# Kernel tuning notes

Hardware: AMD Instinct MI355X
Metric: run time of the kernel (lower is better)

The kernel has to match this reference:

```python
import jax, jax.numpy as jnp
import numpy as np
from jax import lax

EPS = 1e-8
SLOPE = 0.2

def _modconv(x, wv, W, b, sW, sB, demodulate, pad):
    # StyleGAN2 modulated conv, expressed in the equivalent fused form:
    # scale input by per-sample style s, shared-weight conv, then demodulate output.
    s = wv @ sW.T + sB                                   # [B, Cin]
    y = lax.conv_general_dilated(
        x * s[:, :, None, None], W, (1, 1), [(pad, pad), (pad, pad)],
        dimension_numbers=("NCHW", "OIHW", "NCHW"))      # [B, Cout, H, W]
    if demodulate:
        # d[b,o] = 1/sqrt(sum_{i,k,k} (W[o,i,k,k]*s[b,i])^2 + eps)
        d = lax.rsqrt(jnp.einsum("oihw,bi->bo", W * W, s * s) + EPS)
        y = y * d[:, :, None, None]
    return y + b[None, :, None, None]

def _up2(x):
    B, C, H, W = x.shape
    # matches torch F.interpolate(scale_factor=2, mode='bilinear', align_corners=False)
    return jax.image.resize(x, (B, C, 2 * H, 2 * W), method="bilinear")

def setup_inputs() -> dict:
    B, CIN, COUT, NZ, H = 8, 512, 512, 512, 32
    key = jax.random.key(0)
    ks = jax.random.split(key, 20)
    wscale3 = 1.0 / np.sqrt(CIN * 9)   # kaiming-ish equalized-lr scale baked into weights
    wscale1 = 1.0 / np.sqrt(COUT)
    sscale = 1.0 / np.sqrt(NZ)
    return {
        "maps": jax.random.normal(ks[0], (B, CIN, H, H), jnp.float32),
        "w": jax.random.normal(ks[1], (B, NZ), jnp.float32),
        "rgb": jax.random.normal(ks[2], (B, 3, H, H), jnp.float32),
        "noise0": jax.random.normal(ks[3], (B, 1, 2 * H, 2 * H), jnp.float32),
        "noise1": jax.random.normal(ks[4], (B, 1, 2 * H, 2 * H), jnp.float32),
        "w0": jax.random.normal(ks[5], (COUT, CIN, 3, 3), jnp.float32) * wscale3,
        "b0": jnp.zeros((COUT,), jnp.float32),
        "sW0": jax.random.normal(ks[6], (CIN, NZ), jnp.float32) * sscale,
        "sB0": jnp.ones((CIN,), jnp.float32),
        "ns0": jax.random.normal(ks[7], (COUT,), jnp.float32) * 0.1,
        "w1": jax.random.normal(ks[8], (COUT, COUT, 3, 3), jnp.float32) * wscale3,
        "b1": jnp.zeros((COUT,), jnp.float32),
        "sW1": jax.random.normal(ks[9], (COUT, NZ), jnp.float32) * sscale,
        "sB1": jnp.ones((COUT,), jnp.float32),
        "ns1": jax.random.normal(ks[10], (COUT,), jnp.float32) * 0.1,
        "rgbW": jax.random.normal(ks[11], (3, COUT, 1, 1), jnp.float32) * wscale1,
        "rgbB": jnp.zeros((3,), jnp.float32),
        "rgbSW": jax.random.normal(ks[12], (COUT, NZ), jnp.float32) * sscale,
        "rgbSB": jnp.ones((COUT,), jnp.float32),
    }

def reference(maps, w, rgb, noise0, noise1,
              w0, b0, sW0, sB0, ns0,
              w1, b1, sW1, sB1, ns1,
              rgbW, rgbB, rgbSW, rgbSB):
    rgb = _up2(rgb)
    x = _up2(maps)
    # layer 0: modulated conv 3x3 + noise + leakyrelu
    x = _modconv(x, w, w0, b0, sW0, sB0, True, 1)
    x = x + ns0[None, :, None, None] * noise0
    x = jnp.where(x >= 0, x, SLOPE * x)
    # layer 1
    x = _modconv(x, w, w1, b1, sW1, sB1, True, 1)
    x = x + ns1[None, :, None, None] * noise1
    x = jnp.where(x >= 0, x, SLOPE * x)
    # to_rgb: modulated 1x1 conv, no demodulation
    rgb_out = rgb + _modconv(x, w, rgbW, rgbB, rgbSW, rgbSB, False, 0)
    return (rgb_out, x)
```

## Files before the change

### kernel.cpp

```cpp
#include <hip/hip_runtime.h>

typedef unsigned short u16;
typedef short bf16x8 __attribute__((ext_vector_type(8)));
typedef float f32x4 __attribute__((ext_vector_type(4)));
typedef u16 u16x4 __attribute__((ext_vector_type(4)));
typedef u16 u16x8 __attribute__((ext_vector_type(8)));
typedef unsigned u32x4 __attribute__((ext_vector_type(4)));

__device__ __forceinline__ float b2f(u16 v) {
  union { unsigned u; float f; } x; x.u = ((unsigned)v) << 16; return x.f;
}
__device__ __forceinline__ u16 f2b(float f) {
  unsigned u = __float_as_uint(f);
  unsigned r = (u + 0x7FFFu + ((u >> 16) & 1u)) >> 16;
  return (u16)r;
}
__device__ __forceinline__ float rin(const void* p, size_t i, int bf) {
  return bf ? b2f(((const u16*)p)[i]) : ((const float*)p)[i];
}
__device__ __forceinline__ void async16(const void* g, void* l) {
  __builtin_amdgcn_global_load_lds((const __attribute__((address_space(1))) unsigned*)g,
                                   (__attribute__((address_space(3))) unsigned*)l, 16, 0, 0);
}
__device__ __forceinline__ int detect_bf(const unsigned* __restrict__ w0raw, int tid, int* shflag) {
  if (tid < 64) {
    const unsigned lo = w0raw[tid] & 0xFFFFu;
    const unsigned e = (lo >> 7) & 0xFFu;
    const unsigned long long bad = __ballot(e < 100u || e > 126u);
    if (tid == 0) *shflag = (bad == 0ull) ? 1 : 0;
  }
  __syncthreads();
  return *shflag;
}

__global__ void styleall_kernel(const void* __restrict__ w,
                                const void* __restrict__ sW0, const void* __restrict__ sB0,
                                const void* __restrict__ sW1, const void* __restrict__ sB1,
                                const void* __restrict__ sWR, const void* __restrict__ sBR,
                                float* __restrict__ s0, float* __restrict__ s1,
                                float* __restrict__ sR, const unsigned* __restrict__ w0raw) {
  __shared__ int shflag;
  const int tid = threadIdx.x;
  const int bf = detect_bf(w0raw, tid, &shflag);
  const int mat = blockIdx.z, b = blockIdx.y, oc = blockIdx.x;
  const void* sW = (mat == 0) ? sW0 : ((mat == 1) ? sW1 : sWR);
  const void* sB = (mat == 0) ? sB0 : ((mat == 1) ? sB1 : sBR);
  float* out = (mat == 0) ? s0 : ((mat == 1) ? s1 : sR);
  const int i = oc * 64 + (tid >> 2), q = tid & 3;
  float acc = 0.f;
  if (bf) {
    const u16* rp = (const u16*)sW + (size_t)i * 512 + q * 128;
    const u16* wp = (const u16*)w + b * 512 + q * 128;
    for (int z = 0; z < 128; z += 8) {
      u16x8 a = *(const u16x8*)(rp + z), c = *(const u16x8*)(wp + z);
#pragma unroll
      for (int j = 0; j < 8; ++j) acc += b2f(a[j]) * b2f(c[j]);
    }
  } else {
    const float* rp = (const float*)sW + (size_t)i * 512 + q * 128;
    const float* wp = (const float*)w + b * 512 + q * 128;
    for (int z = 0; z < 128; z += 4) {
      f32x4 a = *(const f32x4*)(rp + z), c = *(const f32x4*)(wp + z);
#pragma unroll
      for (int j = 0; j < 4; ++j) acc += a[j] * c[j];
    }
  }
  acc += __shfl_xor(acc, 1, 64);
  acc += __shfl_xor(acc, 2, 64);
  if (q == 0) out[b * 512 + i] = acc + rin(sB, i, bf);
}

__global__ void demod_kernel(const void* __restrict__ W0, const void* __restrict__ W1,
                             const float* __restrict__ s0, const float* __restrict__ s1,
                             float* __restrict__ dm0, float* __restrict__ dm1,
                             u16* __restrict__ Wp0, u16* __restrict__ Wp1,
                             const unsigned* __restrict__ w0raw) {
  __shared__ int shflag;
  __shared__ float wl[4608];
  __shared__ float wsq[512];
  const int tid = threadIdx.x, lane = tid & 63, wv = tid >> 6;
  const int bf = detect_bf(w0raw, tid, &shflag);
  const int o = blockIdx.x, layer = blockIdx.y;
  const void* W = layer ? W1 : W0;
  const float* s = layer ? s1 : s0;
  float* d = layer ? dm1 : dm0;
  u16* Wp = layer ? Wp1 : Wp0;

  if (bf) {
    const u16* src = (const u16*)W + (size_t)o * 4608;
    for (int e = tid; e < 576; e += 256) {
      u16x8 v = *(const u16x8*)(src + e * 8);
#pragma unroll
      for (int j = 0; j < 8; ++j) wl[e * 8 + j] = b2f(v[j]);
    }
  } else {
    const float* src = (const float*)W + (size_t)o * 4608;
    for (int e = tid; e < 1152; e += 256) {
      f32x4 v = *(const f32x4*)(src + e * 4);
#pragma unroll
      for (int j = 0; j < 4; ++j) wl[e * 4 + j] = v[j];
    }
  }
  __syncthreads();
  for (int i = tid; i < 512; i += 256) {
    float ss = 0.f;
#pragma unroll
    for (int t = 0; t < 9; ++t) {
      const float f = wl[i * 9 + t];
      ss += f * f;
      Wp[t * 262144 + o * 512 + i] = f2b(f);
    }
    wsq[i] = ss;
  }
  __syncthreads();
#pragma unroll
  for (int bb = 0; bb < 2; ++bb) {
    const int b = wv * 2 + bb;
    float part = 0.f;
    for (int i = lane; i < 512; i += 64) { const float sv = s[b * 512 + i]; part += wsq[i] * sv * sv; }
#pragma unroll
    for (int st = 1; st < 64; st <<= 1) part += __shfl_xor(part, st, 64);
    if (lane == 0) d[b * 512 + o] = rsqrtf(part + 1e-8f);
  }
}

__global__ void prep_kernel(u16* __restrict__ actB, u32x4* __restrict__ zr, int NB) {
  const int id = blockIdx.x, tid = threadIdx.x;
  if (id < NB * 65) {
    const int bl = id / 65, sub = id - bl * 65;
    const int c = sub * 256 + tid;
    const int px = c >> 6, seg = c & 63;
    int oy, ox;
    if (px < 66)       { oy = 0;  ox = px; }
    else if (px < 132) { oy = 65; ox = px - 66; }
    else { const int e = px - 132; oy = 1 + (e >> 1); ox = (e & 1) * 65; }
    u32x4 z = {0, 0, 0, 0};
    *(u32x4*)&actB[((size_t)(bl * 4356) + oy * 66 + ox) * 512 + seg * 8] = z;
  } else {
    const int c = (id - NB * 65) * 256 + tid;
    if (c < 24832) { u32x4 z = {0, 0, 0, 0}; zr[c] = z; }
  }
}

__global__ void upsample_kernel(const void* __restrict__ maps, const float* __restrict__ s,
                                void* __restrict__ outb, int b_base,
                                const unsigned* __restrict__ w0raw) {
  __shared__ int shflag;
  __shared__ float it[32][2][33];
  const int tid = threadIdx.x;
  const int bf = detect_bf(w0raw, tid, &shflag);
  const size_t esz = bf ? 2 : 4;
  u16* xg = (u16*)((char*)outb + (98304 + (size_t)(b_base >> 2) * 8388608) * esz);
  int oy, i0, bl;
  if (gridDim.z == 8) {
    const int id = blockIdx.x + (blockIdx.y << 6) + (blockIdx.z << 10);
    bl = id & 7; const int r = id >> 3; oy = r & 63; i0 = (r >> 6) << 5;
  } else {
    oy = blockIdx.x; i0 = blockIdx.y << 5; bl = blockIdx.z;
  }
  const int bg = b_base + bl;
  const int m = oy >> 1;
  int iy0, iy1; float wy0, wy1;
  if ((oy & 1) == 0) { iy0 = (m > 0) ? m - 1 : 0; iy1 = m; wy0 = 0.25f; wy1 = 0.75f; }
  else               { iy0 = m; iy1 = (m < 31) ? m + 1 : 31; wy0 = 0.75f; wy1 = 0.25f; }
#pragma unroll
  for (int k = 0; k < 8; ++k) {
    const int e = tid + k * 256;
    const int c = e >> 6, wsel = (e >> 5) & 1, x = e & 31;
    const int iy = wsel ? iy1 : iy0;
    it[c][wsel][x] = rin(maps, ((size_t)(bg * 512 + i0 + c) * 32 + iy) * 32 + x, bf);
  }
  __syncthreads();
#pragma unroll
  for (int k = 0; k < 8; ++k) {
    const int e = tid + k * 256;
    const int xx = e >> 5, c = e & 31;
    const int mx = xx >> 1;
    int ix0, ix1; float wx0, wx1;
    if ((xx & 1) == 0) { ix0 = (mx > 0) ? mx - 1 : 0; ix1 = mx; wx0 = 0.25f; wx1 = 0.75f; }
    else               { ix0 = mx; ix1 = (mx < 31) ? mx + 1 : 31; wx0 = 0.75f; wx1 = 0.25f; }
    const float r0 = wx0 * it[c][0][ix0] + wx1 * it[c][0][ix1];
    const float r1 = wx0 * it[c][1][ix0] + wx1 * it[c][1][ix1];
    const float v = (wy0 * r0 + wy1 * r1) * s[bg * 512 + i0 + c];
    xg[((size_t)(bl * 4096) + oy * 64 + xx) * 512 + i0 + c] = f2b(v);
  }
}

template <int L>
__global__ __launch_bounds__(512, 2) void conv_kernel(
    void* __restrict__ outb, u16* __restrict__ actBp,
    const u16* __restrict__ Wp, const float* __restrict__ dmod,
    const void* __restrict__ bias, const void* __restrict__ nsc,
    const void* __restrict__ noise, const float* __restrict__ saux,
    const u16* __restrict__ zbuf, const void* __restrict__ rgbW,
    float* __restrict__ rgbacc, int b_base,
    const unsigned* __restrict__ w0raw) {
  __shared__ __attribute__((aligned(16))) u16 lds[65536];
  __shared__ float rgbWl[L == 1 ? 1536 : 4];
  __shared__ int shflag;
  const int tid = threadIdx.x, lane = tid & 63, w = tid >> 6;
  const int bf = detect_bf(w0raw, tid, &shflag);
  const size_t esz = bf ? 2 : 4;

  const int lin = blockIdx.x + (blockIdx.y << 4) + (blockIdx.z << 5);
  const int cpx = (int)(gridDim.z << 2);
  const int wg = (lin & 7) * cpx + (lin >> 3);
  const int bl = wg >> 5, rem = wg & 31;
  const int o0 = (rem >> 4) << 8, n0 = (rem & 15) << 8;
  const int bg = b_base + bl;
  const int wm = w >> 2, wn = w & 3;

  if constexpr (L == 1) {
    for (int e = tid; e < 1536; e += 512) rgbWl[e] = rin(rgbW, e, bf);
  }
  const u16* xg = (const u16*)((const char*)outb +
                  (98304 + (size_t)(b_base >> 2) * 8388608) * esz);

  const int q = lane >> 4, m15 = lane & 15;
  const int lro = m15 * 64 + ((q ^ (lane & 7)) * 8);
  const int srow8 = lane >> 3, schunk = (lane & 7) ^ srow8;
  const size_t aAst = (size_t)(o0 + srow8) * 512 + schunk * 8;

  const int ka0 = (w < 4) ? (2 * w) : (16 + 2 * (w - 4));
  const int ka1 = ka0 + 8;
  const int kbe = (w & 3) * 8 + (w >> 2) * 2;
  const int kb0 = kbe, kb1 = kbe + 1, kb2 = kbe + 4, kb3 = kbe + 5;
  int oyv[4], oxv[4];
  size_t pB[4];
  {
    const int kk4[4] = {kb0, kb1, kb2, kb3};
#pragma unroll
    for (int j = 0; j < 4; ++j) {
      const int p = n0 + kk4[j] * 8 + srow8;
      const int oy = p >> 6, ox = p & 63;
      oyv[j] = oy; oxv[j] = ox;
      pB[j] = ((size_t)bl * 4356 + oy * 66 + ox) * 512 + schunk * 8;
    }
  }

  const u16* bBase[4];
  int koff, aoffu;
  auto setTap = [&](int tn_) {
    const int ty_ = (tn_ * 11) >> 5, tx_ = tn_ - ty_ * 3;
    koff = 0;
    aoffu = tn_ * 262144;
    if constexpr (L == 0) {
#pragma unroll
      for (int j = 0; j < 4; ++j) {
        const int iy_ = oyv[j] + ty_ - 1, ix_ = oxv[j] + tx_ - 1;
        bBase[j] = (((unsigned)iy_ < 64u) & ((unsigned)ix_ < 64u))
          ? (xg + ((size_t)((bl << 12) + (iy_ << 6) + ix_) * 512 + schunk * 8))
          : (zbuf + schunk * 8);
      }
    } else {
      const int sb_ = (ty_ * 66 + tx_) * 512;
#pragma unroll
      for (int j = 0; j < 4; ++j) bBase[j] = actBp + pB[j] + sb_;
    }
  };

#define STAGE_A(k_) \
  async16(Wp + aAst + (size_t)aoffu + (size_t)(k_) * 4096, &lds[stb + (k_) * 512])
#define STAGE_B(j_, k_) \
  async16(bBase[j_] + koff, &lds[stb + 16384 + (k_) * 512])

  f32x4 acc[8][4] = {};
  {
    setTap(0);
    const int stb = 0;
    STAGE_A(ka0); STAGE_A(ka0 + 1);
    STAGE_A(ka1); STAGE_A(ka1 + 1);
    STAGE_B(0, kb0); STAGE_B(1, kb1);
    STAGE_B(2, kb2); STAGE_B(3, kb3);
  }
  koff = 64; aoffu = 64;
  asm volatile("s_waitcnt vmcnt(0)" ::: "memory");
  __builtin_amdgcn_s_barrier();

  int arA  = wm * 8192 + lro;
  int arAx = wm * 8192 + (lro ^ 32);
  int arB  = 16384 + wn * 4096 + lro;
  int arBx = 16384 + wn * 4096 + (lro ^ 32);
  int stb  = 32768;

  bf16x8 afr[4][2], bfA[2][2], bfB[2][2];
#pragma unroll 1
  for (int s = 0; s < 72; ++s) {
    const int s1 = s + 1, ok = (s1 < 72);
    if (ok && (s1 & 7) == 0) setTap(s1 >> 3);

#pragma unroll
    for (int mi = 0; mi < 4; ++mi) {
      afr[mi][0] = *(const bf16x8*)&lds[arA + mi * 1024];
      afr[mi][1] = *(const bf16x8*)&lds[arAx + mi * 1024];
    }
#pragma unroll
    for (int ni = 0; ni < 2; ++ni) {
      bfA[ni][0] = *(const bf16x8*)&lds[arB + ni * 1024];
      bfA[ni][1] = *(const bf16x8*)&lds[arBx + ni * 1024];
      bfB[ni][0] = *(const bf16x8*)&lds[arB + 2048 + ni * 1024];
      bfB[ni][1] = *(const bf16x8*)&lds[arBx + 2048 + ni * 1024];
    }
    if (ok) {
      STAGE_A(ka0); STAGE_A(ka0 + 1);
      STAGE_B(0, kb0); STAGE_B(1, kb1);
      STAGE_B(2, kb2); STAGE_B(3, kb3);
    }
    __builtin_amdgcn_s_setprio(1);
#pragma unroll
    for (int mi = 0; mi < 4; ++mi)
#pragma unroll
      for (int ni = 0; ni < 2; ++ni)
#pragma unroll
        for (int kk = 0; kk < 2; ++kk)
          acc[mi][ni] = __builtin_amdgcn_mfma_f32_16x16x32_bf16(
              afr[mi][kk], bfA[ni][kk], acc[mi][ni], 0, 0, 0);
#pragma unroll
    for (int mi = 0; mi < 4; ++mi)
#pragma unroll
      for (int ni = 0; ni < 2; ++ni)
#pragma unroll
        for (int kk = 0; kk < 2; ++kk)
          acc[mi][2 + ni] = __builtin_amdgcn_mfma_f32_16x16x32_bf16(
              afr[mi][kk], bfB[ni][kk], acc[mi][2 + ni], 0, 0, 0);
    __builtin_amdgcn_s_setprio(0);
    if (ok) { asm volatile("s_waitcnt vmcnt(6)" ::: "memory"); }
    else    { asm volatile("s_waitcnt vmcnt(0)" ::: "memory"); }
    __builtin_amdgcn_s_barrier();

#pragma unroll
    for (int mi = 0; mi < 4; ++mi) {
      afr[mi][0] = *(const bf16x8*)&lds[arA + 4096 + mi * 1024];
      afr[mi][1] = *(const bf16x8*)&lds[arAx + 4096 + mi * 1024];
    }
    if (ok) { STAGE_A(ka1); STAGE_A(ka1 + 1); }
    __builtin_amdgcn_s_setprio(1);
#pragma unroll
    for (int mi = 0; mi < 4; ++mi)
#pragma unroll
      for (int ni = 0; ni < 2; ++ni)
#pragma unroll
        for (int kk = 0; kk < 2; ++kk)
          acc[4 + mi][ni] = __builtin_amdgcn_mfma_f32_16x16x32_bf16(
              afr[mi][kk], bfA[ni][kk], acc[4 + mi][ni], 0, 0, 0);
#pragma unroll
    for (int mi = 0; mi < 4; ++mi)
#pragma unroll
      for (int ni = 0; ni < 2; ++ni)
#pragma unroll
        for (int kk = 0; kk < 2; ++kk)
          acc[4 + mi][2 + ni] = __builtin_amdgcn_mfma_f32_16x16x32_bf16(
              afr[mi][kk], bfB[ni][kk], acc[4 + mi][2 + ni], 0, 0, 0);
    __builtin_amdgcn_s_setprio(0);
    if (ok) { asm volatile("s_waitcnt vmcnt(2)" ::: "memory"); }
    __builtin_amdgcn_s_barrier();

    arA ^= 32768; arAx ^= 32768; arB ^= 32768; arBx ^= 32768; stb ^= 32768;
    koff += 64; aoffu += 64;
  }
#undef STAGE_A
#undef STAGE_B

  if constexpr (L == 0) {
#pragma unroll
    for (int ai = 0; ai < 8; ++ai) {
      const int o = o0 + wm * 128 + ai * 16 + q * 4;
      const f32x4 dv = *(const f32x4*)&dmod[bg * 512 + o];
      const f32x4 sv = *(const f32x4*)&saux[bg * 512 + o];
      float bv[4], nv[4];
#pragma unroll
      for (int r = 0; r < 4; ++r) { bv[r] = rin(bias, o + r, bf); nv[r] = rin(nsc, o + r, bf); }
#pragma unroll
      for (int bj = 0; bj < 4; ++bj) {
        const int p = n0 + wn * 64 + bj * 16 + m15;
        const float np = rin(noise, (size_t)bg * 4096 + p, bf);
        u16x4 pack;
#pragma unroll
        for (int r = 0; r < 4; ++r) {
          float v = acc[ai][bj][r] * dv[r] + bv[r] + nv[r] * np;
          v = (v >= 0.f) ? v : 0.2f * v;
          pack[r] = f2b(v * sv[r]);
        }
        const int oy = p >> 6, ox = p & 63;
        *(u16x4*)&actBp[((size_t)(bl * 4356) + (oy + 1) * 66 + (ox + 1)) * 512 + o] = pack;
      }
    }
  } else {
    char* xreg = (char*)outb + 98304 * esz;
    float racc[4][3] = {};
#pragma unroll
    for (int ai = 0; ai < 8; ++ai) {
      const int o = o0 + wm * 128 + ai * 16 + q * 4;
      const f32x4 dv = *(const f32x4*)&dmod[bg * 512 + o];
      const f32x4 srv = *(const f32x4*)&saux[bg * 512 + o];
      float bv[4], nv[4], w0l[4], w1l[4], w2l[4];
#pragma unroll
      for (int r = 0; r < 4; ++r) {
        bv[r] = rin(bias, o + r, bf); nv[r] = rin(nsc, o + r, bf);
        w0l[r] = rgbWl[o + r]; w1l[r] = rgbWl[512 + o + r]; w2l[r] = rgbWl[1024 + o + r];
      }
#pragma unroll
      for (int bj = 0; bj < 4; ++bj) {
        const int p = n0 + wn * 64 + bj * 16 + m15;
        const float np = rin(noise, (size_t)bg * 4096 + p, bf);
#pragma unroll
        for (int r = 0; r < 4; ++r) {
          float v = acc[ai][bj][r] * dv[r] + bv[r] + nv[r] * np;
          v = (v >= 0.f) ? v : 0.2f * v;
          const size_t xi = (size_t)(bg * 512 + o + r) * 4096 + p;
          if (bf) ((u16*)xreg)[xi] = f2b(v); else ((float*)xreg)[xi] = v;
          const float xr = v * srv[r];
          racc[bj][0] += w0l[r] * xr;
          racc[bj][1] += w1l[r] * xr;
          racc[bj][2] += w2l[r] * xr;
        }
      }
    }
#pragma unroll
    for (int bj = 0; bj < 4; ++bj) {
      const int p = n0 + wn * 64 + bj * 16 + m15;
#pragma unroll
      for (int c = 0; c < 3; ++c) {
        float t = racc[bj][c];
        t += __shfl_xor(t, 16, 64);
        t += __shfl_xor(t, 32, 64);
        if (lane < 16) atomicAdd(&rgbacc[(size_t)(bg * 3 + c) * 4096 + p], t);
      }
    }
  }
}

__global__ void rgbfin_kernel(const float* __restrict__ rgbacc, const void* __restrict__ rgbB,
                              const void* __restrict__ rgb, void* __restrict__ outb,
                              const unsigned* __restrict__ w0raw) {
  __shared__ int shflag;
  const int tid = threadIdx.x;
  const int bf = detect_bf(w0raw, tid, &shflag);
  const int g = blockIdx.x * 256 + tid;
  const int b = g >> 12, p = g & 4095;
  const int oy = p >> 6, ox = p & 63;
  const int m = oy >> 1; int iy0, iy1; float wy0, wy1;
  if ((oy & 1) == 0) { iy0 = (m > 0) ? m - 1 : 0; iy1 = m; wy0 = 0.25f; wy1 = 0.75f; }
  else               { iy0 = m; iy1 = (m < 31) ? m + 1 : 31; wy0 = 0.75f; wy1 = 0.25f; }
  const int mx = ox >> 1; int ix0, ix1; float wx0, wx1;
  if ((ox & 1) == 0) { ix0 = (mx > 0) ? mx - 1 : 0; ix1 = mx; wx0 = 0.25f; wx1 = 0.75f; }
  else               { ix0 = mx; ix1 = (mx < 31) ? mx + 1 : 31; wx0 = 0.75f; wx1 = 0.25f; }
#pragma unroll
  for (int c = 0; c < 3; ++c) {
    const size_t rb = (size_t)(b * 3 + c) * 1024;
    const float up = wy0 * (wx0 * rin(rgb, rb + iy0 * 32 + ix0, bf) + wx1 * rin(rgb, rb + iy0 * 32 + ix1, bf))
                   + wy1 * (wx0 * rin(rgb, rb + iy1 * 32 + ix0, bf) + wx1 * rin(rgb, rb + iy1 * 32 + ix1, bf));
    const float v = up + rin(rgbB, c, bf) + rgbacc[(size_t)(b * 3 + c) * 4096 + p];
    const size_t oi = ((size_t)(b * 3 + c) << 12) + p;
    if (bf) ((u16*)outb)[oi] = f2b(v); else ((float*)outb)[oi] = v;
  }
}


extern "C" void kernel_launch(void* const* d_in, const int* in_sizes, int n_in,
                              void* d_out, int out_size, void* d_ws, size_t ws_size,
                              hipStream_t stream) {
  const void* maps   = d_in[0];
  const void* wlat   = d_in[1];
  const void* rgb    = d_in[2];
  const void* noise0 = d_in[3];
  const void* noise1 = d_in[4];
  const void* w0     = d_in[5];
  const void* b0     = d_in[6];
  const void* sW0    = d_in[7];
  const void* sB0    = d_in[8];
  const void* ns0    = d_in[9];
  const void* w1     = d_in[10];
  const void* b1     = d_in[11];
  const void* sW1    = d_in[12];
  const void* sB1    = d_in[13];
  const void* ns1    = d_in[14];
  const void* rgbW   = d_in[15];
  const void* rgbB   = d_in[16];
  const void* rgbSW  = d_in[17];
  const void* rgbSB  = d_in[18];
  const unsigned* w0raw = (const unsigned*)w0;

  char* ws = (char*)d_ws;
  float* s0     = (float*)(ws + 1024);
  float* s1     = (float*)(ws + 17408);
  float* sR     = (float*)(ws + 33792);
  float* dm0    = (float*)(ws + 50176);
  float* dm1    = (float*)(ws + 66560);
  u16*   zbuf   = (u16*)(ws + 82944);
  float* rgbacc = (float*)(ws + 87040);
  u16*   Wp0    = (u16*)(ws + 480256);
  u16*   Wp1    = (u16*)(ws + 5198848);
  u16*   actB   = (u16*)(ws + 9917440);

  const bool full = ws_size >= (size_t)(9917440 + 35684352);
  const int NB = full ? 8 : 4;

  styleall_kernel<<<dim3(8, 8, 3), 256, 0, stream>>>(wlat, sW0, sB0, sW1, sB1, rgbSW, rgbSB,
                                                     s0, s1, sR, w0raw);
  demod_kernel<<<dim3(512, 2), 256, 0, stream>>>(w0, w1, s0, s1, dm0, dm1, Wp0, Wp1, w0raw);
  prep_kernel<<<NB * 65 + 97, 256, 0, stream>>>(actB, (u32x4*)zbuf, NB);

  for (int pass = 0; pass < 8 / NB; ++pass) {
    const int b_base = pass * NB;
    upsample_kernel<<<dim3(64, 16, NB), 256, 0, stream>>>(maps, s0, d_out, b_base, w0raw);
    conv_kernel<0><<<dim3(16, 2, NB), 512, 0, stream>>>(d_out, actB, Wp0, dm0,
        b0, ns0, noise0, s1, zbuf, nullptr, nullptr, b_base, w0raw);
    conv_kernel<1><<<dim3(16, 2, NB), 512, 0, stream>>>(d_out, actB, Wp1, dm1,
        b1, ns1, noise1, sR, zbuf, rgbW, rgbacc, b_base, w0raw);
  }
  rgbfin_kernel<<<128, 256, 0, stream>>>(rgbacc, rgbB, rgb, d_out, w0raw);
}
```

Before: 432.2 us.

## Shrink conv GEMM tiles to 128x128 with 256-thread blocks for more occupancy

The implicit-GEMM conv kernels now use 128x128 output tiles computed by 4 waves instead of 256x256 tiles by 8 waves. The grid grows from 256 to 1024 blocks, with half the LDS per block and reworked staging and wait counts. The goal is better CU load balance and latency hiding from more resident blocks, at the cost of lower data reuse per tile and more global/L2 traffic for weights and activations.

Result: slower. 512.6 us (+18.6%).

```diff
diff --git a/kernel.cpp b/kernel.cpp
--- a/kernel.cpp
+++ b/kernel.cpp
@@ -187,7 +187,7 @@
 }
 
 template <int L>
-__global__ __launch_bounds__(512, 2) void conv_kernel(
+__global__ __launch_bounds__(256, 2) void conv_kernel(
     void* __restrict__ outb, u16* __restrict__ actBp,
     const u16* __restrict__ Wp, const float* __restrict__ dmod,
     const void* __restrict__ bias, const void* __restrict__ nsc,
@@ -195,23 +195,23 @@
     const u16* __restrict__ zbuf, const void* __restrict__ rgbW,
     float* __restrict__ rgbacc, int b_base,
     const unsigned* __restrict__ w0raw) {
-  __shared__ __attribute__((aligned(16))) u16 lds[65536];
+  __shared__ __attribute__((aligned(16))) u16 lds[32768];
   __shared__ float rgbWl[L == 1 ? 1536 : 4];
   __shared__ int shflag;
   const int tid = threadIdx.x, lane = tid & 63, w = tid >> 6;
   const int bf = detect_bf(w0raw, tid, &shflag);
   const size_t esz = bf ? 2 : 4;
 
-  const int lin = blockIdx.x + (blockIdx.y << 4) + (blockIdx.z << 5);
-  const int cpx = (int)(gridDim.z << 2);
+  const int lin = blockIdx.x + (blockIdx.y << 5) + (blockIdx.z << 7);
+  const int cpx = (int)(gridDim.z << 4);
   const int wg = (lin & 7) * cpx + (lin >> 3);
-  const int bl = wg >> 5, rem = wg & 31;
-  const int o0 = (rem >> 4) << 8, n0 = (rem & 15) << 8;
+  const int bl = wg >> 7, rem = wg & 127;
+  const int o0 = (rem >> 5) << 7, n0 = (rem & 31) << 7;
   const int bg = b_base + bl;
-  const int wm = w >> 2, wn = w & 3;
+  const int wm = w >> 1, wn = w & 1;
 
   if constexpr (L == 1) {
-    for (int e = tid; e < 1536; e += 512) rgbWl[e] = rin(rgbW, e, bf);
+    for (int e = tid; e < 1536; e += 256) rgbWl[e] = rin(rgbW, e, bf);
   }
   const u16* xg = (const u16*)((const char*)outb +
                   (98304 + (size_t)(b_base >> 2) * 8388608) * esz);
@@ -221,14 +221,11 @@
   const int srow8 = lane >> 3, schunk = (lane & 7) ^ srow8;
   const size_t aAst = (size_t)(o0 + srow8) * 512 + schunk * 8;
 
-  const int ka0 = (w < 4) ? (2 * w) : (16 + 2 * (w - 4));
-  const int ka1 = ka0 + 8;
-  const int kbe = (w & 3) * 8 + (w >> 2) * 2;
-  const int kb0 = kbe, kb1 = kbe + 1, kb2 = kbe + 4, kb3 = kbe + 5;
+  const int sbase = (w & 1) * 2 + (w >> 1) * 8;
   int oyv[4], oxv[4];
   size_t pB[4];
   {
-    const int kk4[4] = {kb0, kb1, kb2, kb3};
+    const int kk4[4] = {sbase, sbase + 1, sbase + 4, sbase + 5};
 #pragma unroll
     for (int j = 0; j < 4; ++j) {
       const int p = n0 + kk4[j] * 8 + srow8;
@@ -262,100 +259,84 @@
 #define STAGE_A(k_) \
   async16(Wp + aAst + (size_t)aoffu + (size_t)(k_) * 4096, &lds[stb + (k_) * 512])
 #define STAGE_B(j_, k_) \
-  async16(bBase[j_] + koff, &lds[stb + 16384 + (k_) * 512])
-
-  f32x4 acc[8][4] = {};
+  async16(bBase[j_] + koff, &lds[stb + 8192 + (k_) * 512])
+
+  f32x4 acc[4][4] = {};
   {
     setTap(0);
     const int stb = 0;
-    STAGE_A(ka0); STAGE_A(ka0 + 1);
-    STAGE_A(ka1); STAGE_A(ka1 + 1);
-    STAGE_B(0, kb0); STAGE_B(1, kb1);
-    STAGE_B(2, kb2); STAGE_B(3, kb3);
+    STAGE_A(sbase); STAGE_A(sbase + 1);
+    STAGE_A(sbase + 4); STAGE_A(sbase + 5);
+    STAGE_B(0, sbase); STAGE_B(1, sbase + 1);
+    STAGE_B(2, sbase + 4); STAGE_B(3, sbase + 5);
   }
   koff = 64; aoffu = 64;
   asm volatile("s_waitcnt vmcnt(0)" ::: "memory");
   __builtin_amdgcn_s_barrier();
 
-  int arA  = wm * 8192 + lro;
-  int arAx = wm * 8192 + (lro ^ 32);
-  int arB  = 16384 + wn * 4096 + lro;
-  int arBx = 16384 + wn * 4096 + (lro ^ 32);
-  int stb  = 32768;
-
-  bf16x8 afr[4][2], bfA[2][2], bfB[2][2];
+  int arA  = wm * 4096 + lro;
+  int arAx = wm * 4096 + (lro ^ 32);
+  int arB  = 8192 + wn * 4096 + lro;
+  int arBx = 8192 + wn * 4096 + (lro ^ 32);
+  int stb  = 16384;
+
+  bf16x8 afr[2][2], bfr[4][2];
 #pragma unroll 1
   for (int s = 0; s < 72; ++s) {
     const int s1 = s + 1, ok = (s1 < 72);
     if (ok && (s1 & 7) == 0) setTap(s1 >> 3);
 
 #pragma unroll
-    for (int mi = 0; mi < 4; ++mi) {
+    for (int ni = 0; ni < 4; ++ni) {
+      bfr[ni][0] = *(const bf16x8*)&lds[arB + ni * 1024];
+      bfr[ni][1] = *(const bf16x8*)&lds[arBx + ni * 1024];
+    }
+#pragma unroll
+    for (int mi = 0; mi < 2; ++mi) {
       afr[mi][0] = *(const bf16x8*)&lds[arA + mi * 1024];
       afr[mi][1] = *(const bf16x8*)&lds[arAx + mi * 1024];
     }
-#pragma unroll
-    for (int ni = 0; ni < 2; ++ni) {
-      bfA[ni][0] = *(const bf16x8*)&lds[arB + ni * 1024];
-      bfA[ni][1] = *(const bf16x8*)&lds[arBx + ni * 1024];
-      bfB[ni][0] = *(const bf16x8*)&lds[arB + 2048 + ni * 1024];
-      bfB[ni][1] = *(const bf16x8*)&lds[arBx + 2048 + ni * 1024];
-    }
     if (ok) {
-      STAGE_A(ka0); STAGE_A(ka0 + 1);
-      STAGE_B(0, kb0); STAGE_B(1, kb1);
-      STAGE_B(2, kb2); STAGE_B(3, kb3);
+      STAGE_A(sbase); STAGE_A(sbase + 1);
+      STAGE_B(0, sbase); STAGE_B(1, sbase + 1);
     }
     __builtin_amdgcn_s_setprio(1);
 #pragma unroll
-    for (int mi = 0; mi < 4; ++mi)
-#pragma unroll
-      for (int ni = 0; ni < 2; ++ni)
+    for (int mi = 0; mi < 2; ++mi)
+#pragma unroll
+      for (int ni = 0; ni < 4; ++ni)
 #pragma unroll
         for (int kk = 0; kk < 2; ++kk)
           acc[mi][ni] = __builtin_amdgcn_mfma_f32_16x16x32_bf16(
-              afr[mi][kk], bfA[ni][kk], acc[mi][ni], 0, 0, 0);
-#pragma unroll
-    for (int mi = 0; mi < 4; ++mi)
-#pragma unroll
-      for (int ni = 0; ni < 2; ++ni)
-#pragma unroll
-        for (int kk = 0; kk < 2; ++kk)
-          acc[mi][2 + ni] = __builtin_amdgcn_mfma_f32_16x16x32_bf16(
-              afr[mi][kk], bfB[ni][kk], acc[mi][2 + ni], 0, 0, 0);
+              afr[mi][kk], bfr[ni][kk], acc[mi][ni], 0, 0, 0);
     __builtin_amdgcn_s_setprio(0);
-    if (ok) { asm volatile("s_waitcnt vmcnt(6)" ::: "memory"); }
+    if (ok) { asm volatile("s_waitcnt vmcnt(4)" ::: "memory"); }
     else    { asm volatile("s_waitcnt vmcnt(0)" ::: "memory"); }
     __builtin_amdgcn_s_barrier();
 
 #pragma unroll
-    for (int mi = 0; mi < 4; ++mi) {
-      afr[mi][0] = *(const bf16x8*)&lds[arA + 4096 + mi * 1024];
-      afr[mi][1] = *(const bf16x8*)&lds[arAx + 4096 + mi * 1024];
-    }
-    if (ok) { STAGE_A(ka1); STAGE_A(ka1 + 1); }
+    for (int mi = 0; mi < 2; ++mi) {
+      afr[mi][0] = *(const bf16x8*)&lds[arA + 2048 + mi * 1024];
+      afr[mi][1] = *(const bf16x8*)&lds[arAx + 2048 + mi * 1024];
+    }
+    if (ok) {
+      STAGE_B(2, sbase + 4); STAGE_B(3, sbase + 5);
+      STAGE_A(sbase + 4); STAGE_A(sbase + 5);
+    }
     __builtin_amdgcn_s_setprio(1);
 #pragma unroll
-    for (int mi = 0; mi < 4; ++mi)
-#pragma unroll
-      for (int ni = 0; ni < 2; ++ni)
+    for (int mi = 0; mi < 2; ++mi)
+#pragma unroll
+      for (int ni = 0; ni < 4; ++ni)
 #pragma unroll
         for (int kk = 0; kk < 2; ++kk)
-          acc[4 + mi][ni] = __builtin_amdgcn_mfma_f32_16x16x32_bf16(
-              afr[mi][kk], bfA[ni][kk], acc[4 + mi][ni], 0, 0, 0);
-#pragma unroll
-    for (int mi = 0; mi < 4; ++mi)
-#pragma unroll
-      for (int ni = 0; ni < 2; ++ni)
-#pragma unroll
-        for (int kk = 0; kk < 2; ++kk)
-          acc[4 + mi][2 + ni] = __builtin_amdgcn_mfma_f32_16x16x32_bf16(
-              afr[mi][kk], bfB[ni][kk], acc[4 + mi][2 + ni], 0, 0, 0);
+          acc[2 + mi][ni] = __builtin_amdgcn_mfma_f32_16x16x32_bf16(
+              afr[mi][kk], bfr[ni][kk], acc[2 + mi][ni], 0, 0, 0);
     __builtin_amdgcn_s_setprio(0);
     if (ok) { asm volatile("s_waitcnt vmcnt(2)" ::: "memory"); }
     __builtin_amdgcn_s_barrier();
 
-    arA ^= 32768; arAx ^= 32768; arB ^= 32768; arBx ^= 32768; stb ^= 32768;
+    arA ^= 16384; arAx ^= 16384; arB ^= 16384; arBx ^= 16384; stb ^= 16384;
     koff += 64; aoffu += 64;
   }
 #undef STAGE_A
@@ -363,8 +344,8 @@
 
   if constexpr (L == 0) {
 #pragma unroll
-    for (int ai = 0; ai < 8; ++ai) {
-      const int o = o0 + wm * 128 + ai * 16 + q * 4;
+    for (int ai = 0; ai < 4; ++ai) {
+      const int o = o0 + wm * 64 + ai * 16 + q * 4;
       const f32x4 dv = *(const f32x4*)&dmod[bg * 512 + o];
       const f32x4 sv = *(const f32x4*)&saux[bg * 512 + o];
       float bv[4], nv[4];
@@ -389,8 +370,8 @@
     char* xreg = (char*)outb + 98304 * esz;
     float racc[4][3] = {};
 #pragma unroll
-    for (int ai = 0; ai < 8; ++ai) {
-      const int o = o0 + wm * 128 + ai * 16 + q * 4;
+    for (int ai = 0; ai < 4; ++ai) {
+      const int o = o0 + wm * 64 + ai * 16 + q * 4;
       const f32x4 dv = *(const f32x4*)&dmod[bg * 512 + o];
       const f32x4 srv = *(const f32x4*)&saux[bg * 512 + o];
       float bv[4], nv[4], w0l[4], w1l[4], w2l[4];
@@ -504,9 +485,9 @@
   for (int pass = 0; pass < 8 / NB; ++pass) {
     const int b_base = pass * NB;
     upsample_kernel<<<dim3(64, 16, NB), 256, 0, stream>>>(maps, s0, d_out, b_base, w0raw);
-    conv_kernel<0><<<dim3(16, 2, NB), 512, 0, stream>>>(d_out, actB, Wp0, dm0,
+    conv_kernel<0><<<dim3(32, 4, NB), 256, 0, stream>>>(d_out, actB, Wp0, dm0,
         b0, ns0, noise0, s1, zbuf, nullptr, nullptr, b_base, w0raw);
-    conv_kernel<1><<<dim3(16, 2, NB), 512, 0, stream>>>(d_out, actB, Wp1, dm1,
+    conv_kernel<1><<<dim3(32, 4, NB), 256, 0, stream>>>(d_out, actB, Wp1, dm1,
         b1, ns1, noise1, sR, zbuf, rgbW, rgbacc, b_base, w0raw);
   }
   rgbfin_kernel<<<128, 256, 0, stream>>>(rgbacc, rgbB, rgb, d_out, w0raw);
```

## Switch conv GEMM main loop from 16x16x32 to 32x32x16 MFMA tiles

Applied to the files above, without the earlier changes.

Replaces the 16x16x32 bf16 MFMA micro-tiling with 32x32x16 MFMA instructions that accumulate into 16-wide vectors. LDS fragment reads, the swizzled column offsets, the waitcnt counts and both epilogues (layer-0 activation write and layer-1 x/rgb accumulation) are remapped to the new accumulator layout. The larger MFMA shape is meant to cut LDS reads and instruction count per FLOP. It changes the swizzle read pattern, so it risks LDS bank conflicts and higher register pressure.

Result: slower. 556.0 us (+28.6%).

```diff
diff --git a/kernel.cpp b/kernel.cpp
--- a/kernel.cpp
+++ b/kernel.cpp
@@ -3,6 +3,7 @@
 typedef unsigned short u16;
 typedef short bf16x8 __attribute__((ext_vector_type(8)));
 typedef float f32x4 __attribute__((ext_vector_type(4)));
+typedef float f32x16 __attribute__((ext_vector_type(16)));
 typedef u16 u16x4 __attribute__((ext_vector_type(4)));
 typedef u16 u16x8 __attribute__((ext_vector_type(8)));
 typedef unsigned u32x4 __attribute__((ext_vector_type(4)));
@@ -216,8 +217,10 @@
   const u16* xg = (const u16*)((const char*)outb +
                   (98304 + (size_t)(b_base >> 2) * 8388608) * esz);
 
-  const int q = lane >> 4, m15 = lane & 15;
-  const int lro = m15 * 64 + ((q ^ (lane & 7)) * 8);
+  const int h = lane >> 5, l7 = lane & 7, l31 = lane & 31;
+  int co[4];
+#pragma unroll
+  for (int kq = 0; kq < 4; ++kq) co[kq] = ((((kq << 1) | h) ^ l7) << 3);
   const int srow8 = lane >> 3, schunk = (lane & 7) ^ srow8;
   const size_t aAst = (size_t)(o0 + srow8) * 512 + schunk * 8;
 
@@ -264,7 +267,7 @@
 #define STAGE_B(j_, k_) \
   async16(bBase[j_] + koff, &lds[stb + 16384 + (k_) * 512])
 
-  f32x4 acc[8][4] = {};
+  f32x16 acc[4][2] = {};
   {
     setTap(0);
     const int stb = 0;
@@ -277,29 +280,25 @@
   asm volatile("s_waitcnt vmcnt(0)" ::: "memory");
   __builtin_amdgcn_s_barrier();
 
-  int arA  = wm * 8192 + lro;
-  int arAx = wm * 8192 + (lro ^ 32);
-  int arB  = 16384 + wn * 4096 + lro;
-  int arBx = 16384 + wn * 4096 + (lro ^ 32);
-  int stb  = 32768;
-
-  bf16x8 afr[4][2], bfA[2][2], bfB[2][2];
+  int arA = wm * 8192 + l31 * 64;
+  int arB = 16384 + wn * 4096 + l31 * 64;
+  int stb = 32768;
+
+  bf16x8 afr[2][4], bfr[2][4];
 #pragma unroll 1
   for (int s = 0; s < 72; ++s) {
     const int s1 = s + 1, ok = (s1 < 72);
     if (ok && (s1 & 7) == 0) setTap(s1 >> 3);
 
 #pragma unroll
-    for (int mi = 0; mi < 4; ++mi) {
-      afr[mi][0] = *(const bf16x8*)&lds[arA + mi * 1024];
-      afr[mi][1] = *(const bf16x8*)&lds[arAx + mi * 1024];
-    }
-#pragma unroll
-    for (int ni = 0; ni < 2; ++ni) {
-      bfA[ni][0] = *(const bf16x8*)&lds[arB + ni * 1024];
-      bfA[ni][1] = *(const bf16x8*)&lds[arBx + ni * 1024];
-      bfB[ni][0] = *(const bf16x8*)&lds[arB + 2048 + ni * 1024];
-      bfB[ni][1] = *(const bf16x8*)&lds[arBx + 2048 + ni * 1024];
+    for (int kq = 0; kq < 4; ++kq) {
+      bfr[0][kq] = *(const bf16x8*)&lds[arB + co[kq]];
+      bfr[1][kq] = *(const bf16x8*)&lds[arB + 2048 + co[kq]];
+    }
+#pragma unroll
+    for (int kq = 0; kq < 4; ++kq) {
+      afr[0][kq] = *(const bf16x8*)&lds[arA + co[kq]];
+      afr[1][kq] = *(const bf16x8*)&lds[arA + 2048 + co[kq]];
     }
     if (ok) {
       STAGE_A(ka0); STAGE_A(ka0 + 1);
@@ -308,54 +307,38 @@
     }
     __builtin_amdgcn_s_setprio(1);
 #pragma unroll
-    for (int mi = 0; mi < 4; ++mi)
-#pragma unroll
-      for (int ni = 0; ni < 2; ++ni)
-#pragma unroll
-        for (int kk = 0; kk < 2; ++kk)
-          acc[mi][ni] = __builtin_amdgcn_mfma_f32_16x16x32_bf16(
-              afr[mi][kk], bfA[ni][kk], acc[mi][ni], 0, 0, 0);
-#pragma unroll
-    for (int mi = 0; mi < 4; ++mi)
-#pragma unroll
-      for (int ni = 0; ni < 2; ++ni)
-#pragma unroll
-        for (int kk = 0; kk < 2; ++kk)
-          acc[mi][2 + ni] = __builtin_amdgcn_mfma_f32_16x16x32_bf16(
-              afr[mi][kk], bfB[ni][kk], acc[mi][2 + ni], 0, 0, 0);
+    for (int kq = 0; kq < 4; ++kq)
+#pragma unroll
+      for (int mi = 0; mi < 2; ++mi)
+#pragma unroll
+        for (int ni = 0; ni < 2; ++ni)
+          acc[mi][ni] = __builtin_amdgcn_mfma_f32_32x32x16_bf16(
+              afr[mi][kq], bfr[ni][kq], acc[mi][ni], 0, 0, 0);
     __builtin_amdgcn_s_setprio(0);
-    if (ok) { asm volatile("s_waitcnt vmcnt(6)" ::: "memory"); }
+    if (ok) { asm volatile("s_waitcnt vmcnt(4)" ::: "memory"); }
     else    { asm volatile("s_waitcnt vmcnt(0)" ::: "memory"); }
     __builtin_amdgcn_s_barrier();
 
 #pragma unroll
-    for (int mi = 0; mi < 4; ++mi) {
-      afr[mi][0] = *(const bf16x8*)&lds[arA + 4096 + mi * 1024];
-      afr[mi][1] = *(const bf16x8*)&lds[arAx + 4096 + mi * 1024];
+    for (int kq = 0; kq < 4; ++kq) {
+      afr[0][kq] = *(const bf16x8*)&lds[arA + 4096 + co[kq]];
+      afr[1][kq] = *(const bf16x8*)&lds[arA + 6144 + co[kq]];
     }
     if (ok) { STAGE_A(ka1); STAGE_A(ka1 + 1); }
     __builtin_amdgcn_s_setprio(1);
 #pragma unroll
-    for (int mi = 0; mi < 4; ++mi)
-#pragma unroll
-      for (int ni = 0; ni < 2; ++ni)
-#pragma unroll
-        for (int kk = 0; kk < 2; ++kk)
-          acc[4 + mi][ni] = __builtin_amdgcn_mfma_f32_16x16x32_bf16(
-              afr[mi][kk], bfA[ni][kk], acc[4 + mi][ni], 0, 0, 0);
-#pragma unroll
-    for (int mi = 0; mi < 4; ++mi)
-#pragma unroll
-      for (int ni = 0; ni < 2; ++ni)
-#pragma unroll
-        for (int kk = 0; kk < 2; ++kk)
-          acc[4 + mi][2 + ni] = __builtin_amdgcn_mfma_f32_16x16x32_bf16(
-              afr[mi][kk], bfB[ni][kk], acc[4 + mi][2 + ni], 0, 0, 0);
+    for (int kq = 0; kq < 4; ++kq)
+#pragma unroll
+      for (int mi = 0; mi < 2; ++mi)
+#pragma unroll
+        for (int ni = 0; ni < 2; ++ni)
+          acc[2 + mi][ni] = __builtin_amdgcn_mfma_f32_32x32x16_bf16(
+              afr[mi][kq], bfr[ni][kq], acc[2 + mi][ni], 0, 0, 0);
     __builtin_amdgcn_s_setprio(0);
     if (ok) { asm volatile("s_waitcnt vmcnt(2)" ::: "memory"); }
     __builtin_amdgcn_s_barrier();
 
-    arA ^= 32768; arAx ^= 32768; arB ^= 32768; arBx ^= 32768; stb ^= 32768;
+    arA ^= 32768; arB ^= 32768; stb ^= 32768;
     koff += 64; aoffu += 64;
   }
 #undef STAGE_A
@@ -363,68 +346,79 @@
 
   if constexpr (L == 0) {
 #pragma unroll
-    for (int ai = 0; ai < 8; ++ai) {
-      const int o = o0 + wm * 128 + ai * 16 + q * 4;
-      const f32x4 dv = *(const f32x4*)&dmod[bg * 512 + o];
-      const f32x4 sv = *(const f32x4*)&saux[bg * 512 + o];
-      float bv[4], nv[4];
-#pragma unroll
-      for (int r = 0; r < 4; ++r) { bv[r] = rin(bias, o + r, bf); nv[r] = rin(nsc, o + r, bf); }
-#pragma unroll
-      for (int bj = 0; bj < 4; ++bj) {
-        const int p = n0 + wn * 64 + bj * 16 + m15;
+    for (int mi = 0; mi < 4; ++mi) {
+      f32x4 dvv[4], svv[4]; float bvv[4][4], nvv[4][4];
+#pragma unroll
+      for (int g = 0; g < 4; ++g) {
+        const int o = o0 + wm * 128 + mi * 32 + g * 8 + h * 4;
+        dvv[g] = *(const f32x4*)&dmod[bg * 512 + o];
+        svv[g] = *(const f32x4*)&saux[bg * 512 + o];
+#pragma unroll
+        for (int r = 0; r < 4; ++r) { bvv[g][r] = rin(bias, o + r, bf); nvv[g][r] = rin(nsc, o + r, bf); }
+      }
+#pragma unroll
+      for (int ni = 0; ni < 2; ++ni) {
+        const int p = n0 + wn * 64 + ni * 32 + l31;
         const float np = rin(noise, (size_t)bg * 4096 + p, bf);
-        u16x4 pack;
-#pragma unroll
-        for (int r = 0; r < 4; ++r) {
-          float v = acc[ai][bj][r] * dv[r] + bv[r] + nv[r] * np;
-          v = (v >= 0.f) ? v : 0.2f * v;
-          pack[r] = f2b(v * sv[r]);
+        const int oy = p >> 6, ox = p & 63;
+        u16* wbase = &actBp[((size_t)(bl * 4356) + (oy + 1) * 66 + (ox + 1)) * 512];
+#pragma unroll
+        for (int g = 0; g < 4; ++g) {
+          const int o = o0 + wm * 128 + mi * 32 + g * 8 + h * 4;
+          u16x4 pack;
+#pragma unroll
+          for (int r = 0; r < 4; ++r) {
+            float v = acc[mi][ni][g * 4 + r] * dvv[g][r] + bvv[g][r] + nvv[g][r] * np;
+            v = (v >= 0.f) ? v : 0.2f * v;
+            pack[r] = f2b(v * svv[g][r]);
+          }
+          *(u16x4*)&wbase[o] = pack;
         }
-        const int oy = p >> 6, ox = p & 63;
-        *(u16x4*)&actBp[((size_t)(bl * 4356) + (oy + 1) * 66 + (ox + 1)) * 512 + o] = pack;
       }
     }
   } else {
     char* xreg = (char*)outb + 98304 * esz;
-    float racc[4][3] = {};
-#pragma unroll
-    for (int ai = 0; ai < 8; ++ai) {
-      const int o = o0 + wm * 128 + ai * 16 + q * 4;
-      const f32x4 dv = *(const f32x4*)&dmod[bg * 512 + o];
-      const f32x4 srv = *(const f32x4*)&saux[bg * 512 + o];
-      float bv[4], nv[4], w0l[4], w1l[4], w2l[4];
-#pragma unroll
-      for (int r = 0; r < 4; ++r) {
-        bv[r] = rin(bias, o + r, bf); nv[r] = rin(nsc, o + r, bf);
-        w0l[r] = rgbWl[o + r]; w1l[r] = rgbWl[512 + o + r]; w2l[r] = rgbWl[1024 + o + r];
+    float racc[2][3] = {};
+#pragma unroll
+    for (int mi = 0; mi < 4; ++mi) {
+      f32x4 dvv[4], srv[4]; float bvv[4][4], nvv[4][4];
+#pragma unroll
+      for (int g = 0; g < 4; ++g) {
+        const int o = o0 + wm * 128 + mi * 32 + g * 8 + h * 4;
+        dvv[g] = *(const f32x4*)&dmod[bg * 512 + o];
+        srv[g] = *(const f32x4*)&saux[bg * 512 + o];
+#pragma unroll
+        for (int r = 0; r < 4; ++r) { bvv[g][r] = rin(bias, o + r, bf); nvv[g][r] = rin(nsc, o + r, bf); }
       }
 #pragma unroll
-      for (int bj = 0; bj < 4; ++bj) {
-        const int p = n0 + wn * 64 + bj * 16 + m15;
+      for (int ni = 0; ni < 2; ++ni) {
+        const int p = n0 + wn * 64 + ni * 32 + l31;
         const float np = rin(noise, (size_t)bg * 4096 + p, bf);
 #pragma unroll
-        for (int r = 0; r < 4; ++r) {
-          float v = acc[ai][bj][r] * dv[r] + bv[r] + nv[r] * np;
-          v = (v >= 0.f) ? v : 0.2f * v;
-          const size_t xi = (size_t)(bg * 512 + o + r) * 4096 + p;
-          if (bf) ((u16*)xreg)[xi] = f2b(v); else ((float*)xreg)[xi] = v;
-          const float xr = v * srv[r];
-          racc[bj][0] += w0l[r] * xr;
-          racc[bj][1] += w1l[r] * xr;
-          racc[bj][2] += w2l[r] * xr;
+        for (int g = 0; g < 4; ++g) {
+          const int o = o0 + wm * 128 + mi * 32 + g * 8 + h * 4;
+#pragma unroll
+          for (int r = 0; r < 4; ++r) {
+            float v = acc[mi][ni][g * 4 + r] * dvv[g][r] + bvv[g][r] + nvv[g][r] * np;
+            v = (v >= 0.f) ? v : 0.2f * v;
+            const size_t xi = (size_t)(bg * 512 + o + r) * 4096 + p;
+            if (bf) ((u16*)xreg)[xi] = f2b(v); else ((float*)xreg)[xi] = v;
+            const float xr = v * srv[g][r];
+            racc[ni][0] += rgbWl[o + r] * xr;
+            racc[ni][1] += rgbWl[512 + o + r] * xr;
+            racc[ni][2] += rgbWl[1024 + o + r] * xr;
+          }
         }
       }
     }
 #pragma unroll
-    for (int bj = 0; bj < 4; ++bj) {
-      const int p = n0 + wn * 64 + bj * 16 + m15;
+    for (int ni = 0; ni < 2; ++ni) {
+      const int p = n0 + wn * 64 + ni * 32 + l31;
 #pragma unroll
       for (int c = 0; c < 3; ++c) {
-        float t = racc[bj][c];
-        t += __shfl_xor(t, 16, 64);
+        float t = racc[ni][c];
         t += __shfl_xor(t, 32, 64);
-        if (lane < 16) atomicAdd(&rgbacc[(size_t)(bg * 3 + c) * 4096 + p], t);
+        if (lane < 32) atomicAdd(&rgbacc[(size_t)(bg * 3 + c) * 4096 + p], t);
       }
     }
   }
```

## Load conv weight fragments directly from global memory, staging only activations in LDS

Applied to the files above, without the earlier changes.

The weight (A) operand is no longer staged through LDS. Each wave loads its MFMA A fragments straight from global memory (L2-cached weights), and only the activation tile is double-buffered in LDS, which halves LDS use and drops one barrier per step. The aim is to cut LDS traffic and synchronisation and possibly raise occupancy. The cost is that global-load latency now sits directly in front of the MFMAs, and the 16-byte fragment loads are only partly coalesced, with just a vmcnt(0) wait protecting them.

Result: slower. 824.6 us (+90.8%).

```diff
diff --git a/kernel.cpp b/kernel.cpp
--- a/kernel.cpp
+++ b/kernel.cpp
@@ -195,7 +195,7 @@
     const u16* __restrict__ zbuf, const void* __restrict__ rgbW,
     float* __restrict__ rgbacc, int b_base,
     const unsigned* __restrict__ w0raw) {
-  __shared__ __attribute__((aligned(16))) u16 lds[65536];
+  __shared__ __attribute__((aligned(16))) u16 lds[32768];
   __shared__ float rgbWl[L == 1 ? 1536 : 4];
   __shared__ int shflag;
   const int tid = threadIdx.x, lane = tid & 63, w = tid >> 6;
@@ -219,10 +219,9 @@
   const int q = lane >> 4, m15 = lane & 15;
   const int lro = m15 * 64 + ((q ^ (lane & 7)) * 8);
   const int srow8 = lane >> 3, schunk = (lane & 7) ^ srow8;
-  const size_t aAst = (size_t)(o0 + srow8) * 512 + schunk * 8;
-
-  const int ka0 = (w < 4) ? (2 * w) : (16 + 2 * (w - 4));
-  const int ka1 = ka0 + 8;
+
+  const u16* aG = Wp + (size_t)(o0 + wm * 128 + m15) * 512 + q * 8;
+
   const int kbe = (w & 3) * 8 + (w >> 2) * 2;
   const int kb0 = kbe, kb1 = kbe + 1, kb2 = kbe + 4, kb3 = kbe + 5;
   int oyv[4], oxv[4];
@@ -239,11 +238,10 @@
   }
 
   const u16* bBase[4];
-  int koff, aoffu;
+  int koff;
   auto setTap = [&](int tn_) {
     const int ty_ = (tn_ * 11) >> 5, tx_ = tn_ - ty_ * 3;
     koff = 0;
-    aoffu = tn_ * 262144;
     if constexpr (L == 0) {
 #pragma unroll
       for (int j = 0; j < 4; ++j) {
@@ -259,106 +257,95 @@
     }
   };
 
-#define STAGE_A(k_) \
-  async16(Wp + aAst + (size_t)aoffu + (size_t)(k_) * 4096, &lds[stb + (k_) * 512])
 #define STAGE_B(j_, k_) \
-  async16(bBase[j_] + koff, &lds[stb + 16384 + (k_) * 512])
+  async16(bBase[j_] + koff, &lds[stb + (k_) * 512])
 
   f32x4 acc[8][4] = {};
+  int stb = 0;
   {
     setTap(0);
-    const int stb = 0;
-    STAGE_A(ka0); STAGE_A(ka0 + 1);
-    STAGE_A(ka1); STAGE_A(ka1 + 1);
     STAGE_B(0, kb0); STAGE_B(1, kb1);
     STAGE_B(2, kb2); STAGE_B(3, kb3);
   }
-  koff = 64; aoffu = 64;
+  koff = 64;
   asm volatile("s_waitcnt vmcnt(0)" ::: "memory");
   __builtin_amdgcn_s_barrier();
 
-  int arA  = wm * 8192 + lro;
-  int arAx = wm * 8192 + (lro ^ 32);
-  int arB  = 16384 + wn * 4096 + lro;
-  int arBx = 16384 + wn * 4096 + (lro ^ 32);
-  int stb  = 32768;
-
-  bf16x8 afr[4][2], bfA[2][2], bfB[2][2];
+  int arB  = wn * 4096 + lro;
+  int arBx = wn * 4096 + (lro ^ 32);
+  stb = 16384;
+
+  bf16x8 afr0[4], afr1[4], bfr[4][2];
 #pragma unroll 1
   for (int s = 0; s < 72; ++s) {
     const int s1 = s + 1, ok = (s1 < 72);
     if (ok && (s1 & 7) == 0) setTap(s1 >> 3);
-
-#pragma unroll
-    for (int mi = 0; mi < 4; ++mi) {
-      afr[mi][0] = *(const bf16x8*)&lds[arA + mi * 1024];
-      afr[mi][1] = *(const bf16x8*)&lds[arAx + mi * 1024];
-    }
-#pragma unroll
-    for (int ni = 0; ni < 2; ++ni) {
-      bfA[ni][0] = *(const bf16x8*)&lds[arB + ni * 1024];
-      bfA[ni][1] = *(const bf16x8*)&lds[arBx + ni * 1024];
-      bfB[ni][0] = *(const bf16x8*)&lds[arB + 2048 + ni * 1024];
-      bfB[ni][1] = *(const bf16x8*)&lds[arBx + 2048 + ni * 1024];
-    }
+    const int aCur = (s >> 3) * 262144 + (s & 7) * 64;
+
+#pragma unroll
+    for (int mi = 0; mi < 4; ++mi)
+      afr0[mi] = *(const bf16x8*)(aG + aCur + mi * 8192);
+#pragma unroll
+    for (int mi = 0; mi < 4; ++mi)
+      afr1[mi] = *(const bf16x8*)(aG + aCur + mi * 8192 + 32);
+
+#pragma unroll
+    for (int ni = 0; ni < 4; ++ni) {
+      bfr[ni][0] = *(const bf16x8*)&lds[arB + ni * 1024];
+      bfr[ni][1] = *(const bf16x8*)&lds[arBx + ni * 1024];
+    }
+
     if (ok) {
-      STAGE_A(ka0); STAGE_A(ka0 + 1);
       STAGE_B(0, kb0); STAGE_B(1, kb1);
       STAGE_B(2, kb2); STAGE_B(3, kb3);
     }
+
     __builtin_amdgcn_s_setprio(1);
 #pragma unroll
     for (int mi = 0; mi < 4; ++mi)
 #pragma unroll
-      for (int ni = 0; ni < 2; ++ni)
-#pragma unroll
-        for (int kk = 0; kk < 2; ++kk)
-          acc[mi][ni] = __builtin_amdgcn_mfma_f32_16x16x32_bf16(
-              afr[mi][kk], bfA[ni][kk], acc[mi][ni], 0, 0, 0);
-#pragma unroll
-    for (int mi = 0; mi < 4; ++mi)
-#pragma unroll
-      for (int ni = 0; ni < 2; ++ni)
-#pragma unroll
-        for (int kk = 0; kk < 2; ++kk)
-          acc[mi][2 + ni] = __builtin_amdgcn_mfma_f32_16x16x32_bf16(
-              afr[mi][kk], bfB[ni][kk], acc[mi][2 + ni], 0, 0, 0);
+      for (int ni = 0; ni < 4; ++ni)
+        acc[mi][ni] = __builtin_amdgcn_mfma_f32_16x16x32_bf16(
+            afr0[mi], bfr[ni][0], acc[mi][ni], 0, 0, 0);
     __builtin_amdgcn_s_setprio(0);
-    if (ok) { asm volatile("s_waitcnt vmcnt(6)" ::: "memory"); }
-    else    { asm volatile("s_waitcnt vmcnt(0)" ::: "memory"); }
-    __builtin_amdgcn_s_barrier();
-
-#pragma unroll
-    for (int mi = 0; mi < 4; ++mi) {
-      afr[mi][0] = *(const bf16x8*)&lds[arA + 4096 + mi * 1024];
-      afr[mi][1] = *(const bf16x8*)&lds[arAx + 4096 + mi * 1024];
-    }
-    if (ok) { STAGE_A(ka1); STAGE_A(ka1 + 1); }
+#pragma unroll
+    for (int mi = 0; mi < 4; ++mi)
+      afr0[mi] = *(const bf16x8*)(aG + aCur + (4 + mi) * 8192);
+
     __builtin_amdgcn_s_setprio(1);
 #pragma unroll
     for (int mi = 0; mi < 4; ++mi)
 #pragma unroll
-      for (int ni = 0; ni < 2; ++ni)
-#pragma unroll
-        for (int kk = 0; kk < 2; ++kk)
-          acc[4 + mi][ni] = __builtin_amdgcn_mfma_f32_16x16x32_bf16(
-              afr[mi][kk], bfA[ni][kk], acc[4 + mi][ni], 0, 0, 0);
-#pragma unroll
-    for (int mi = 0; mi < 4; ++mi)
-#pragma unroll
-      for (int ni = 0; ni < 2; ++ni)
-#pragma unroll
-        for (int kk = 0; kk < 2; ++kk)
-          acc[4 + mi][2 + ni] = __builtin_amdgcn_mfma_f32_16x16x32_bf16(
-              afr[mi][kk], bfB[ni][kk], acc[4 + mi][2 + ni], 0, 0, 0);
+      for (int ni = 0; ni < 4; ++ni)
+        acc[mi][ni] = __builtin_amdgcn_mfma_f32_16x16x32_bf16(
+            afr1[mi], bfr[ni][1], acc[mi][ni], 0, 0, 0);
     __builtin_amdgcn_s_setprio(0);
-    if (ok) { asm volatile("s_waitcnt vmcnt(2)" ::: "memory"); }
-    __builtin_amdgcn_s_barrier();
-
-    arA ^= 32768; arAx ^= 32768; arB ^= 32768; arBx ^= 32768; stb ^= 32768;
-    koff += 64; aoffu += 64;
-  }
-#undef STAGE_A
+#pragma unroll
+    for (int mi = 0; mi < 4; ++mi)
+      afr1[mi] = *(const bf16x8*)(aG + aCur + (4 + mi) * 8192 + 32);
+
+    __builtin_amdgcn_s_setprio(1);
+#pragma unroll
+    for (int mi = 0; mi < 4; ++mi)
+#pragma unroll
+      for (int ni = 0; ni < 4; ++ni)
+        acc[4 + mi][ni] = __builtin_amdgcn_mfma_f32_16x16x32_bf16(
+            afr0[mi], bfr[ni][0], acc[4 + mi][ni], 0, 0, 0);
+#pragma unroll
+    for (int mi = 0; mi < 4; ++mi)
+#pragma unroll
+      for (int ni = 0; ni < 4; ++ni)
+        acc[4 + mi][ni] = __builtin_amdgcn_mfma_f32_16x16x32_bf16(
+            afr1[mi], bfr[ni][1], acc[4 + mi][ni], 0, 0, 0);
+    __builtin_amdgcn_s_setprio(0);
+
+    if (ok) {
+      asm volatile("s_waitcnt vmcnt(0)" ::: "memory");
+      __builtin_amdgcn_s_barrier();
+    }
+    arB ^= 16384; arBx ^= 16384; stb ^= 16384;
+    koff += 64;
+  }
 #undef STAGE_B
 
   if constexpr (L == 0) {
```
